# Kernel optimization log

Hardware: AMD Instinct MI355X
Metric: run time of the kernel (lower is better)

Reference implementation:

```python
import jax, jax.numpy as jnp
import numpy as np

THRESHOLD = 0.1


def _conv3x3(x, w, b):
    # x: [B,Ci,H,W], w: [Co,Ci,3,3] -> [B,Co,H,W], SAME padding, ReLU
    y = jax.lax.conv_general_dilated(
        x, w, window_strides=(1, 1), padding='SAME',
        dimension_numbers=('NCHW', 'OIHW', 'NCHW'))
    return jax.nn.relu(y + b[None, :, None, None])


def _autoencoder(x, w1, b1, w2, b2, w3, b3, w4, b4):
    h = _conv3x3(x, w1, b1)          # 64 -> 32
    mid = _conv3x3(h, w2, b2)        # 32 -> 16 (bottleneck)
    h2 = _conv3x3(mid, w3, b3)       # 16 -> 32
    rec = _conv3x3(h2, w4, b4)       # 32 -> 64
    return mid, rec


def setup_inputs() -> dict:
    key = jax.random.key(0)
    ks = jax.random.split(key, 8)
    B, C, H, W = 8, 64, 128, 256
    s = 0.05  # keep activations / singular values at a sane scale
    return {
        'feat0': jax.random.normal(ks[0], (B, C, H, W), jnp.float32),
        'feat1': jax.random.normal(ks[1], (B, C, H, W), jnp.float32),
        'w1': jax.random.normal(ks[2], (32, 64, 3, 3), jnp.float32) * s,
        'b1': jnp.zeros((32,), jnp.float32),
        'w2': jax.random.normal(ks[3], (16, 32, 3, 3), jnp.float32) * s,
        'b2': jnp.zeros((16,), jnp.float32),
        'w3': jax.random.normal(ks[4], (32, 16, 3, 3), jnp.float32) * s,
        'b3': jnp.zeros((32,), jnp.float32),
        'w4': jax.random.normal(ks[5], (64, 32, 3, 3), jnp.float32) * s,
        'b4': jnp.zeros((64,), jnp.float32),
        'modality_adapter': 0,  # accepted but unused by the original forward
    }


def reference(feat0, feat1, w1, b1, w2, b2, w3, b3, w4, b4, modality_adapter):
    feats = [feat0, feat1]
    B, C, H, W = feat0.shape
    auto_enc_loss = jnp.float32(0.0)
    counts_list = []
    for f in feats:
        mid, rec = _autoencoder(f, w1, b1, w2, b2, w3, b3, w4, b4)
        # batched SVD over [B, 16, H*W]; counts of singular values > threshold
        sv = jnp.linalg.svd(jax.lax.stop_gradient(mid.reshape(B, mid.shape[1], H * W)),
                            compute_uv=False)  # [B, 16]
        counts_list.append(jnp.sum(sv > THRESHOLD, axis=1))
        auto_enc_loss = auto_enc_loss + jnp.mean((f - rec) ** 2)
    # pick the dominant modality per batch element
    domain_idx = jnp.argmax(jnp.stack(counts_list, axis=1), axis=1)  # [B]
    con_feat = jnp.stack(feats, axis=1)                              # [B,M,C,H,W]
    dom = con_feat[jnp.arange(B), domain_idx]                        # [B,C,H,W]
    domain_features = jnp.broadcast_to(dom[:, None], con_feat.shape)  # repeat over M
    # two-stage cross-modal einsum attention
    weights = jnp.einsum('smchw,snchw->smnhw', domain_features, con_feat)
    weights = jax.nn.softmax(weights, axis=2)
    weights = jnp.einsum('smnhw,snchw->smchw', weights, con_feat)
    weights = jax.nn.softmax(weights, axis=1)
    fused_feat = jnp.sum(con_feat * weights, axis=1)  # [B,C,H,W]
    return fused_feat, auto_enc_loss
```

## Files before the change

### kernel.cpp

```cpp
#include <hip/hip_runtime.h>
#include <hip/hip_bf16.h>

#define B_ 8
#define H_ 128
#define W_ 256
#define PH 130
#define PW 258
#define NPIX (B_*64*H_*W_)

typedef short short8  __attribute__((ext_vector_type(8)));
typedef short short4v __attribute__((ext_vector_type(4)));
typedef float floatx4 __attribute__((ext_vector_type(4)));

template<int Ci, int Co, bool LOSS, bool NCHW_IN, bool AVG>
__global__ __launch_bounds__(256)
void conv_mfma(const void* __restrict__ in_,
               const __hip_bfloat16* __restrict__ wt,
               const float* __restrict__ bias,
               __hip_bfloat16* __restrict__ outp,
               const float* __restrict__ ref,
               const float* __restrict__ other,
               float* __restrict__ avg_out,
               float* __restrict__ acc_out)
{
    constexpr int CC   = (Ci >= 32) ? Ci/32 : 1;
    constexpr int PXB  = Ci*2;
    constexpr int NCB  = PXB/16;
    constexpr int SLAB = 6*66*PXB;
    constexpr int NT   = Co/16;
    constexpr int GNT  = (NT >= 2) ? 2 : 1;
    constexpr int NG   = NT / GNT;
    constexpr int EPIW = 64*(Co+8)*2;
    constexpr int RECB = 64*272*2;
    constexpr int LDSZ = LOSS ? (RECB > SLAB ? RECB : SLAB)
                              : (4*EPIW > SLAB ? 4*EPIW : SLAB);
    __shared__ alignas(16) char slab[LDSZ + 32];
    __shared__ float wred[4];

    const int tid  = threadIdx.x;
    const int lane = tid & 63;
    const int wid  = tid >> 6;
    const int col  = lane & 15;
    const int quad = lane >> 4;
    const int w0   = blockIdx.x * 64;
    const int h0   = blockIdx.y * 4;
    const int bz   = blockIdx.z;
    const int r    = wid;

    floatx4 acc[4][NT];
#pragma unroll
    for (int mt = 0; mt < 4; ++mt)
#pragma unroll
        for (int nt = 0; nt < NT; ++nt)
            acc[mt][nt] = (floatx4)0.f;

    if constexpr (NCHW_IN) {
        static_assert(Ci == 64, "NCHW staging is Ci=64 only");
        const float* src = (const float*)in_ + (size_t)bz * 64 * H_ * W_;
        for (int k = tid; k < 8*396; k += 256) {
            int cb  = k / 396;
            int pxl = k - cb*396;
            int row = pxl / 66;
            int pxc = pxl - row*66;
            int gh  = h0 + row - 1;
            int gw  = w0 + pxc - 1;
            bool ok = ((unsigned)gh < (unsigned)H_) && ((unsigned)gw < (unsigned)W_);
            const float* sp = src + (size_t)(cb*8)*(H_*W_)
                              + (size_t)(ok ? gh : 0)*W_ + (ok ? gw : 0);
            short8 v;
#pragma unroll
            for (int j = 0; j < 8; ++j) {
                float f = sp[(size_t)j*(H_*W_)];
                f = ok ? f : 0.f;
                v[j] = __builtin_bit_cast(short, __float2bfloat16(f));
            }
            *(short8*)(slab + pxl*PXB + ((cb ^ (pxl & 7)) << 4)) = v;
        }
    } else {
        const __hip_bfloat16* inb = (const __hip_bfloat16*)in_ + (size_t)bz * PH * PW * Ci;
        for (int o = tid*16; o < SLAB; o += 4096) {
            int pxl = o / PXB;
            int row = pxl / 66;
            int pxc = pxl - row*66;
            int cb  = (o >> 4) & (NCB-1);
            short8 v = *(const short8*)(inb + ((size_t)(h0+row)*PW + (w0+pxc))*Ci + cb*8);
            *(short8*)(slab + pxl*PXB + ((cb ^ (pxl & (NCB-1))) << 4)) = v;
        }
    }
    __syncthreads();

    if constexpr (Ci >= 32) {
#pragma unroll
        for (int c2 = 0; c2 < CC; ++c2) {
#pragma unroll
            for (int g = 0; g < NG; ++g) {
                short8 bfr[9*GNT];
#pragma unroll
                for (int t = 0; t < 9; ++t)
#pragma unroll
                    for (int j = 0; j < GNT; ++j)
                        bfr[t*GNT+j] = *(const short8*)(wt
                            + ((size_t)(c2*9+t)*Co + (g*GNT+j)*16 + col)*32 + quad*8);
#pragma unroll
                for (int t = 0; t < 9; ++t) {
                    const int dy = t/3, dx = t - (t/3)*3;
                    short8 a[4];
#pragma unroll
                    for (int mt = 0; mt < 4; ++mt) {
                        int px = (r+dy)*66 + mt*16 + col + dx;
                        a[mt] = *(const short8*)(slab + px*PXB
                                  + (((c2*4 + quad) ^ (px & (NCB-1))) << 4));
                    }
#pragma unroll
                    for (int j = 0; j < GNT; ++j)
#pragma unroll
                        for (int mt = 0; mt < 4; ++mt)
                            acc[mt][g*GNT+j] = __builtin_amdgcn_mfma_f32_16x16x32_bf16(
                                a[mt], bfr[t*GNT+j], acc[mt][g*GNT+j], 0, 0, 0);
                }
            }
        }
    } else {
        short8 bfr[6*NT];
#pragma unroll
        for (int kc = 0; kc < 6; ++kc)
#pragma unroll
            for (int j = 0; j < NT; ++j)
                bfr[kc*NT+j] = *(const short8*)(wt
                    + ((size_t)kc*Co + j*16 + col)*32 + quad*8);
#pragma unroll
        for (int kc = 0; kc < 6; ++kc) {
            const int dy = kc >> 1, half = kc & 1;
            const int dxe = half ? 2 : (quad >> 1);
            short8 a[4];
#pragma unroll
            for (int mt = 0; mt < 4; ++mt) {
                int px = (r+dy)*66 + mt*16 + col + dxe;
                a[mt] = *(const short8*)(slab + px*PXB
                          + (((quad & 1) ^ (px & 1)) << 4));
            }
#pragma unroll
            for (int j = 0; j < NT; ++j)
#pragma unroll
                for (int mt = 0; mt < 4; ++mt)
                    acc[mt][j] = __builtin_amdgcn_mfma_f32_16x16x32_bf16(
                        a[mt], bfr[kc*NT+j], acc[mt][j], 0, 0, 0);
        }
    }

    if constexpr (!LOSS) {
        __syncthreads();
        char* rt = slab + wid * EPIW;
#pragma unroll
        for (int nt = 0; nt < NT; ++nt) {
            float bv = bias[nt*16 + col];
#pragma unroll
            for (int mt = 0; mt < 4; ++mt) {
#pragma unroll
                for (int rr = 0; rr < 4; ++rr) {
                    float v = acc[mt][nt][rr] + bv;
                    v = v > 0.f ? v : 0.f;
                    int px = mt*16 + quad*4 + rr;
                    *(__hip_bfloat16*)(rt + (px*(Co+8) + nt*16 + col)*2) =
                        __float2bfloat16(v);
                }
            }
        }
        char* grow = (char*)outp
            + (((size_t)bz*PH + (h0 + r + 1))*PW + (w0 + 1))*Co*2;
        constexpr int GB = 64*Co*2;
#pragma unroll
        for (int id = 0; id < GB/1024; ++id) {
            int o  = id*1024 + lane*16;
            int px = o / (Co*2);
            int cb = o - px*(Co*2);
            *(short8*)(grow + o) = *(const short8*)(rt + px*(Co+8)*2 + cb);
        }
    } else {
        __syncthreads();
        __hip_bfloat16* rec = (__hip_bfloat16*)slab;
#pragma unroll
        for (int nt = 0; nt < NT; ++nt) {
            int co = nt*16 + col;
            float bv = bias[co];
#pragma unroll
            for (int mt = 0; mt < 4; ++mt) {
                short4v pk;
#pragma unroll
                for (int rr = 0; rr < 4; ++rr) {
                    float v = acc[mt][nt][rr] + bv;
                    v = v > 0.f ? v : 0.f;
                    pk[rr] = __builtin_bit_cast(short, __float2bfloat16(v));
                }
                *(short4v*)(rec + co*272 + r*68 + mt*16 + quad*4) = pk;
            }
        }
        __syncthreads();

        float lsum = 0.f;
        const float* refb = ref + (size_t)bz * 64 * H_ * W_;
#pragma unroll
        for (int i = 0; i < 16; ++i) {
            int row = i & 3, cg = i >> 2;
            int co  = cg*16 + wid*4 + quad;
            size_t off = ((size_t)co*H_ + h0 + row)*W_ + w0 + col*4;
            float4 f = *(const float4*)(refb + off);
            short4v pk = *(const short4v*)(rec + co*272 + row*68 + col*4);
            float d0 = f.x - __bfloat162float(__builtin_bit_cast(__hip_bfloat16, pk[0]));
            float d1 = f.y - __bfloat162float(__builtin_bit_cast(__hip_bfloat16, pk[1]));
            float d2 = f.z - __bfloat162float(__builtin_bit_cast(__hip_bfloat16, pk[2]));
            float d3 = f.w - __bfloat162float(__builtin_bit_cast(__hip_bfloat16, pk[3]));
            lsum += d0*d0 + d1*d1 + d2*d2 + d3*d3;
            if constexpr (AVG) {
                const float* othb = other + (size_t)bz * 64 * H_ * W_;
                float*       avgb = avg_out + (size_t)bz * 64 * H_ * W_;
                float4 g = *(const float4*)(othb + off);
                float4 o;
                o.x = 0.5f*(f.x + g.x);
                o.y = 0.5f*(f.y + g.y);
                o.z = 0.5f*(f.z + g.z);
                o.w = 0.5f*(f.w + g.w);
                *(float4*)(avgb + off) = o;
            }
        }
#pragma unroll
        for (int off = 32; off > 0; off >>= 1)
            lsum += __shfl_down(lsum, off, 64);
        if (lane == 0) wred[wid] = lsum;
        __syncthreads();
        if (tid == 0)
            atomicAdd(acc_out, (wred[0] + wred[1] + wred[2] + wred[3])
                               * (1.0f / (float)NPIX));
    }
}

template<int C>
__device__ __forceinline__ void zb_item(__hip_bfloat16* buf, int idx)
{
    constexpr int CP = C/8;
    int cb   = idx % CP;
    int cell = (idx / CP) % 772;
    int img  = idx / (CP*772);
    int row, colp;
    if (cell < 258)      { row = 0;   colp = cell; }
    else if (cell < 516) { row = 129; colp = cell - 258; }
    else { int r2 = cell - 516; row = 1 + (r2 >> 1); colp = (r2 & 1) ? 257 : 0; }
    short8 z = (short8)0;
    *(short8*)(buf + (((size_t)img*PH + row)*PW + colp)*C + cb*8) = z;
}

template<int Ci, int Co>
__device__ __forceinline__ void wt_item(const float* __restrict__ w,
                                        __hip_bfloat16* __restrict__ wt, int idx)
{
    int kl = idx & 31;
    int co = (idx >> 5) % Co;
    int kc = idx / (32*Co);
    float val = 0.f;
    if constexpr (Ci >= 32) {
        int c2 = kc / 9, t = kc % 9;
        int dy = t/3, dx = t%3;
        int ci = c2*32 + kl;
        val = w[((size_t)(co*Ci + ci)*3 + dy)*3 + dx];
    } else {
        int dy = kc >> 1, half = kc & 1;
        int dx = half*2 + (kl >> 4);
        int ci = kl & 15;
        if (dx < 3) val = w[((size_t)(co*Ci + ci)*3 + dy)*3 + dx];
    }
    wt[idx] = __float2bfloat16(val);
}

__global__ __launch_bounds__(256)
void setup_kernel(const float* __restrict__ w1, const float* __restrict__ w2,
                  const float* __restrict__ w3, const float* __restrict__ w4,
                  __hip_bfloat16* WT1, __hip_bfloat16* WT2,
                  __hip_bfloat16* WT3, __hip_bfloat16* WT4,
                  __hip_bfloat16* BUF1, __hip_bfloat16* BUF2,
                  float* acc)
{
    int idx = blockIdx.x*256 + threadIdx.x;
    if (idx == 0) *acc = 0.f;
    if      (idx < 24704) zb_item<32>(BUF1, idx);
    else if (idx < 37056) zb_item<16>(BUF2, idx - 24704);
    else if (idx < 55488) wt_item<64,32>(w1, WT1, idx - 37056);
    else if (idx < 60096) wt_item<32,16>(w2, WT2, idx - 55488);
    else if (idx < 66240) wt_item<16,32>(w3, WT3, idx - 60096);
    else if (idx < 84672) wt_item<32,64>(w4, WT4, idx - 66240);
}

__global__ __launch_bounds__(256)
void fused_avg_kernel(const float4* __restrict__ a, const float4* __restrict__ b,
                      float4* __restrict__ o, int n4)
{
    int i = blockIdx.x*256 + threadIdx.x;
    if (i < n4) {
        float4 x = a[i], y = b[i];
        float4 r;
        r.x = 0.5f*(x.x + y.x);
        r.y = 0.5f*(x.y + y.y);
        r.z = 0.5f*(x.z + y.z);
        r.w = 0.5f*(x.w + y.w);
        o[i] = r;
    }
}

extern "C" void kernel_launch(void* const* d_in, const int* in_sizes, int n_in,
                              void* d_out, int out_size, void* d_ws, size_t ws_size,
                              hipStream_t stream)
{
    const float* feat0 = (const float*)d_in[0];
    const float* feat1 = (const float*)d_in[1];
    const float* w1 = (const float*)d_in[2];
    const float* b1 = (const float*)d_in[3];
    const float* w2 = (const float*)d_in[4];
    const float* b2 = (const float*)d_in[5];
    const float* w3 = (const float*)d_in[6];
    const float* b3 = (const float*)d_in[7];
    const float* w4 = (const float*)d_in[8];
    const float* b4 = (const float*)d_in[9];

    float* out = (float*)d_out;
    float* acc = out + NPIX;

    constexpr size_t SCR_SZ = 25853952;
    const bool use_ws = (d_ws != nullptr) && (ws_size >= SCR_SZ);
    char* sb = use_ws ? (char*)d_ws : (char*)d_out;

    __hip_bfloat16* BUF1 = (__hip_bfloat16*)(sb + 0);
    __hip_bfloat16* BUF2 = (__hip_bfloat16*)(sb + 17172480);
    __hip_bfloat16* WT1  = (__hip_bfloat16*)(sb + 25758720);
    __hip_bfloat16* WT2  = (__hip_bfloat16*)(sb + 25795584);
    __hip_bfloat16* WT3  = (__hip_bfloat16*)(sb + 25804800);
    __hip_bfloat16* WT4  = (__hip_bfloat16*)(sb + 25817088);

    setup_kernel<<<331, 256, 0, stream>>>(w1, w2, w3, w4,
                                          WT1, WT2, WT3, WT4, BUF1, BUF2, acc);

    dim3 cgrid(W_/64, H_/4, B_);
    dim3 blk(256);

    const float* feats[2] = { feat0, feat1 };
    for (int m = 0; m < 2; ++m) {
        conv_mfma<64,32,false,true ,false><<<cgrid, blk, 0, stream>>>(
            feats[m], WT1, b1, BUF1, nullptr, nullptr, nullptr, nullptr);
        conv_mfma<32,16,false,false,false><<<cgrid, blk, 0, stream>>>(
            BUF1, WT2, b2, BUF2, nullptr, nullptr, nullptr, nullptr);
        conv_mfma<16,32,false,false,false><<<cgrid, blk, 0, stream>>>(
            BUF2, WT3, b3, BUF1, nullptr, nullptr, nullptr, nullptr);
        if (m == 1 && use_ws)
            conv_mfma<32,64,true ,false,true ><<<cgrid, blk, 0, stream>>>(
                BUF1, WT4, b4, nullptr, feats[1], feats[0], out, acc);
        else
            conv_mfma<32,64,true ,false,false><<<cgrid, blk, 0, stream>>>(
                BUF1, WT4, b4, nullptr, feats[m], nullptr, nullptr, acc);
    }

    if (!use_ws) {
        int n4 = NPIX/4;
        fused_avg_kernel<<<(n4 + 255)/256, 256, 0, stream>>>(
            (const float4*)feat0, (const float4*)feat1, (float4*)out, n4);
    }
}
```

Measured before the change: 340.9 us.

## Batch both modalities into single conv launches and stage NCHW input in channel halves

Both feature maps now go through each conv layer in one launch, with the grid z dimension doubled to 2*B and separate per-modality scratch buffers. This halves the number of kernel launches and gives each launch twice as many blocks, which should fill the GPU better. The first conv also stages its fp32 NCHW input in two 32-channel halves. Each wave loads 8 channels, so the LDS slab is halved and occupancy may rise, at the cost of an extra barrier. Workspace size doubles, and the averaging output is written only by the modality-1 blocks.

```diff
diff --git a/kernel.cpp b/kernel.cpp
--- a/kernel.cpp
+++ b/kernel.cpp
@@ -14,17 +14,21 @@
 
 template<int Ci, int Co, bool LOSS, bool NCHW_IN, bool AVG>
 __global__ __launch_bounds__(256)
-void conv_mfma(const void* __restrict__ in_,
+void conv_mfma(const void* __restrict__ inA,
+               const void* __restrict__ inB,
                const __hip_bfloat16* __restrict__ wt,
                const float* __restrict__ bias,
                __hip_bfloat16* __restrict__ outp,
-               const float* __restrict__ ref,
+               size_t out_mstride,
+               const float* __restrict__ ref0,
+               const float* __restrict__ ref1,
                const float* __restrict__ other,
                float* __restrict__ avg_out,
                float* __restrict__ acc_out)
 {
     constexpr int CC   = (Ci >= 32) ? Ci/32 : 1;
-    constexpr int PXB  = Ci*2;
+    constexpr int SCI  = NCHW_IN ? 32 : Ci;
+    constexpr int PXB  = SCI*2;
     constexpr int NCB  = PXB/16;
     constexpr int SLAB = 6*66*PXB;
     constexpr int NT   = Co/16;
@@ -44,7 +48,9 @@
     const int quad = lane >> 4;
     const int w0   = blockIdx.x * 64;
     const int h0   = blockIdx.y * 4;
-    const int bz   = blockIdx.z;
+    const int zz   = blockIdx.z;
+    const int bz   = zz & 7;
+    const int mz   = zz >> 3;
     const int r    = wid;
 
     floatx4 acc[4][NT];
@@ -54,30 +60,70 @@
         for (int nt = 0; nt < NT; ++nt)
             acc[mt][nt] = (floatx4)0.f;
 
+    auto mfma_c2 = [&](int c2) {
+#pragma unroll
+        for (int g = 0; g < NG; ++g) {
+            short8 bfr[9*GNT];
+#pragma unroll
+            for (int t = 0; t < 9; ++t)
+#pragma unroll
+                for (int j = 0; j < GNT; ++j)
+                    bfr[t*GNT+j] = *(const short8*)(wt
+                        + ((size_t)(c2*9+t)*Co + (g*GNT+j)*16 + col)*32 + quad*8);
+#pragma unroll
+            for (int t = 0; t < 9; ++t) {
+                const int dy = t/3, dx = t - (t/3)*3;
+                short8 a[4];
+#pragma unroll
+                for (int mt = 0; mt < 4; ++mt) {
+                    int px  = (r+dy)*66 + mt*16 + col + dx;
+                    int kch = NCHW_IN ? quad : (c2*4 + quad);
+                    a[mt] = *(const short8*)(slab + px*PXB
+                              + ((kch ^ (px & (NCB-1))) << 4));
+                }
+#pragma unroll
+                for (int j = 0; j < GNT; ++j)
+#pragma unroll
+                    for (int mt = 0; mt < 4; ++mt)
+                        acc[mt][g*GNT+j] = __builtin_amdgcn_mfma_f32_16x16x32_bf16(
+                            a[mt], bfr[t*GNT+j], acc[mt][g*GNT+j], 0, 0, 0);
+            }
+        }
+    };
+
     if constexpr (NCHW_IN) {
         static_assert(Ci == 64, "NCHW staging is Ci=64 only");
-        const float* src = (const float*)in_ + (size_t)bz * 64 * H_ * W_;
-        for (int k = tid; k < 8*396; k += 256) {
-            int cb  = k / 396;
-            int pxl = k - cb*396;
-            int row = pxl / 66;
-            int pxc = pxl - row*66;
-            int gh  = h0 + row - 1;
-            int gw  = w0 + pxc - 1;
-            bool ok = ((unsigned)gh < (unsigned)H_) && ((unsigned)gw < (unsigned)W_);
-            const float* sp = src + (size_t)(cb*8)*(H_*W_)
-                              + (size_t)(ok ? gh : 0)*W_ + (ok ? gw : 0);
-            short8 v;
-#pragma unroll
-            for (int j = 0; j < 8; ++j) {
-                float f = sp[(size_t)j*(H_*W_)];
-                f = ok ? f : 0.f;
-                v[j] = __builtin_bit_cast(short, __float2bfloat16(f));
-            }
-            *(short8*)(slab + pxl*PXB + ((cb ^ (pxl & 7)) << 4)) = v;
+        const float* src = (const float*)(mz ? inB : inA) + (size_t)bz * 64 * H_ * W_;
+#pragma unroll
+        for (int c2 = 0; c2 < CC; ++c2) {
+            if (c2) __syncthreads();
+            const float* chb = src + (size_t)(c2*32 + wid*8) * (H_*W_);
+#pragma unroll
+            for (int it = 0; it < 7; ++it) {
+                int pxl = it*64 + lane;
+                bool live = (it < 6) || (lane < 12);
+                int row = pxl / 66;
+                int pxc = pxl - row*66;
+                int gh  = h0 + row - 1;
+                int gw  = w0 + pxc - 1;
+                bool ok = live && ((unsigned)gh < (unsigned)H_)
+                               && ((unsigned)gw < (unsigned)W_);
+                const float* sp = chb + (size_t)(ok ? gh : 0)*W_ + (ok ? gw : 0);
+                short8 v;
+#pragma unroll
+                for (int j = 0; j < 8; ++j) {
+                    float f = sp[(size_t)j*(H_*W_)];
+                    v[j] = __builtin_bit_cast(short, __float2bfloat16(ok ? f : 0.f));
+                }
+                if (live)
+                    *(short8*)(slab + pxl*PXB + ((wid ^ (pxl & (NCB-1))) << 4)) = v;
+            }
+            __syncthreads();
+            mfma_c2(c2);
         }
     } else {
-        const __hip_bfloat16* inb = (const __hip_bfloat16*)in_ + (size_t)bz * PH * PW * Ci;
+        const __hip_bfloat16* inb = (const __hip_bfloat16*)(mz ? inB : inA)
+                                    + (size_t)bz * PH * PW * Ci;
         for (int o = tid*16; o < SLAB; o += 4096) {
             int pxl = o / PXB;
             int row = pxl / 66;
@@ -86,65 +132,38 @@
             short8 v = *(const short8*)(inb + ((size_t)(h0+row)*PW + (w0+pxc))*Ci + cb*8);
             *(short8*)(slab + pxl*PXB + ((cb ^ (pxl & (NCB-1))) << 4)) = v;
         }
-    }
-    __syncthreads();
-
-    if constexpr (Ci >= 32) {
-#pragma unroll
-        for (int c2 = 0; c2 < CC; ++c2) {
-#pragma unroll
-            for (int g = 0; g < NG; ++g) {
-                short8 bfr[9*GNT];
-#pragma unroll
-                for (int t = 0; t < 9; ++t)
-#pragma unroll
-                    for (int j = 0; j < GNT; ++j)
-                        bfr[t*GNT+j] = *(const short8*)(wt
-                            + ((size_t)(c2*9+t)*Co + (g*GNT+j)*16 + col)*32 + quad*8);
-#pragma unroll
-                for (int t = 0; t < 9; ++t) {
-                    const int dy = t/3, dx = t - (t/3)*3;
-                    short8 a[4];
-#pragma unroll
-                    for (int mt = 0; mt < 4; ++mt) {
-                        int px = (r+dy)*66 + mt*16 + col + dx;
-                        a[mt] = *(const short8*)(slab + px*PXB
-                                  + (((c2*4 + quad) ^ (px & (NCB-1))) << 4));
-                    }
-#pragma unroll
-                    for (int j = 0; j < GNT; ++j)
-#pragma unroll
-                        for (int mt = 0; mt < 4; ++mt)
-                            acc[mt][g*GNT+j] = __builtin_amdgcn_mfma_f32_16x16x32_bf16(
-                                a[mt], bfr[t*GNT+j], acc[mt][g*GNT+j], 0, 0, 0);
-                }
-            }
-        }
-    } else {
-        short8 bfr[6*NT];
-#pragma unroll
-        for (int kc = 0; kc < 6; ++kc)
-#pragma unroll
-            for (int j = 0; j < NT; ++j)
-                bfr[kc*NT+j] = *(const short8*)(wt
-                    + ((size_t)kc*Co + j*16 + col)*32 + quad*8);
-#pragma unroll
-        for (int kc = 0; kc < 6; ++kc) {
-            const int dy = kc >> 1, half = kc & 1;
-            const int dxe = half ? 2 : (quad >> 1);
-            short8 a[4];
-#pragma unroll
-            for (int mt = 0; mt < 4; ++mt) {
-                int px = (r+dy)*66 + mt*16 + col + dxe;
-                a[mt] = *(const short8*)(slab + px*PXB
-                          + (((quad & 1) ^ (px & 1)) << 4));
-            }
-#pragma unroll
-            for (int j = 0; j < NT; ++j)
-#pragma unroll
-                for (int mt = 0; mt < 4; ++mt)
-                    acc[mt][j] = __builtin_amdgcn_mfma_f32_16x16x32_bf16(
-                        a[mt], bfr[kc*NT+j], acc[mt][j], 0, 0, 0);
+        __syncthreads();
+
+        if constexpr (Ci >= 32) {
+#pragma unroll
+            for (int c2 = 0; c2 < CC; ++c2)
+                mfma_c2(c2);
+        } else {
+            short8 bfr[6*NT];
+#pragma unroll
+            for (int kc = 0; kc < 6; ++kc)
+#pragma unroll
+                for (int j = 0; j < NT; ++j)
+                    bfr[kc*NT+j] = *(const short8*)(wt
+                        + ((size_t)kc*Co + j*16 + col)*32 + quad*8);
+#pragma unroll
+            for (int kc = 0; kc < 6; ++kc) {
+                const int dy = kc >> 1, half = kc & 1;
+                const int dxe = half ? 2 : (quad >> 1);
+                short8 a[4];
+#pragma unroll
+                for (int mt = 0; mt < 4; ++mt) {
+                    int px = (r+dy)*66 + mt*16 + col + dxe;
+                    a[mt] = *(const short8*)(slab + px*PXB
+                              + (((quad & 1) ^ (px & 1)) << 4));
+                }
+#pragma unroll
+                for (int j = 0; j < NT; ++j)
+#pragma unroll
+                    for (int mt = 0; mt < 4; ++mt)
+                        acc[mt][j] = __builtin_amdgcn_mfma_f32_16x16x32_bf16(
+                            a[mt], bfr[kc*NT+j], acc[mt][j], 0, 0, 0);
+            }
         }
     }
 
@@ -166,7 +185,8 @@
                 }
             }
         }
-        char* grow = (char*)outp
+        __hip_bfloat16* ob = outp + (size_t)mz * out_mstride;
+        char* grow = (char*)ob
             + (((size_t)bz*PH + (h0 + r + 1))*PW + (w0 + 1))*Co*2;
         constexpr int GB = 64*Co*2;
 #pragma unroll
@@ -198,7 +218,7 @@
         __syncthreads();
 
         float lsum = 0.f;
-        const float* refb = ref + (size_t)bz * 64 * H_ * W_;
+        const float* refb = (mz ? ref1 : ref0) + (size_t)bz * 64 * H_ * W_;
 #pragma unroll
         for (int i = 0; i < 16; ++i) {
             int row = i & 3, cg = i >> 2;
@@ -212,15 +232,17 @@
             float d3 = f.w - __bfloat162float(__builtin_bit_cast(__hip_bfloat16, pk[3]));
             lsum += d0*d0 + d1*d1 + d2*d2 + d3*d3;
             if constexpr (AVG) {
-                const float* othb = other + (size_t)bz * 64 * H_ * W_;
-                float*       avgb = avg_out + (size_t)bz * 64 * H_ * W_;
-                float4 g = *(const float4*)(othb + off);
-                float4 o;
-                o.x = 0.5f*(f.x + g.x);
-                o.y = 0.5f*(f.y + g.y);
-                o.z = 0.5f*(f.z + g.z);
-                o.w = 0.5f*(f.w + g.w);
-                *(float4*)(avgb + off) = o;
+                if (mz) {
+                    const float* othb = other + (size_t)bz * 64 * H_ * W_;
+                    float*       avgb = avg_out + (size_t)bz * 64 * H_ * W_;
+                    float4 g = *(const float4*)(othb + off);
+                    float4 o;
+                    o.x = 0.5f*(f.x + g.x);
+                    o.y = 0.5f*(f.y + g.y);
+                    o.z = 0.5f*(f.z + g.z);
+                    o.w = 0.5f*(f.w + g.w);
+                    *(float4*)(avgb + off) = o;
+                }
             }
         }
 #pragma unroll
@@ -281,12 +303,12 @@
 {
     int idx = blockIdx.x*256 + threadIdx.x;
     if (idx == 0) *acc = 0.f;
-    if      (idx < 24704) zb_item<32>(BUF1, idx);
-    else if (idx < 37056) zb_item<16>(BUF2, idx - 24704);
-    else if (idx < 55488) wt_item<64,32>(w1, WT1, idx - 37056);
-    else if (idx < 60096) wt_item<32,16>(w2, WT2, idx - 55488);
-    else if (idx < 66240) wt_item<16,32>(w3, WT3, idx - 60096);
-    else if (idx < 84672) wt_item<32,64>(w4, WT4, idx - 66240);
+    if      (idx <  49408) zb_item<32>(BUF1, idx);
+    else if (idx <  74112) zb_item<16>(BUF2, idx - 49408);
+    else if (idx <  92544) wt_item<64,32>(w1, WT1, idx - 74112);
+    else if (idx <  97152) wt_item<32,16>(w2, WT2, idx - 92544);
+    else if (idx < 103296) wt_item<16,32>(w3, WT3, idx - 97152);
+    else if (idx < 121728) wt_item<32,64>(w4, WT4, idx - 103296);
 }
 
 __global__ __launch_bounds__(256)
@@ -323,40 +345,45 @@
     float* out = (float*)d_out;
     float* acc = out + NPIX;
 
-    constexpr size_t SCR_SZ = 25853952;
+    constexpr size_t B1B = (size_t)B_*PH*PW*32*2;
+    constexpr size_t B2B = (size_t)B_*PH*PW*16*2;
+    constexpr size_t SCR_SZ = 51612672;
     const bool use_ws = (d_ws != nullptr) && (ws_size >= SCR_SZ);
     char* sb = use_ws ? (char*)d_ws : (char*)d_out;
 
     __hip_bfloat16* BUF1 = (__hip_bfloat16*)(sb + 0);
-    __hip_bfloat16* BUF2 = (__hip_bfloat16*)(sb + 17172480);
-    __hip_bfloat16* WT1  = (__hip_bfloat16*)(sb + 25758720);
-    __hip_bfloat16* WT2  = (__hip_bfloat16*)(sb + 25795584);
-    __hip_bfloat16* WT3  = (__hip_bfloat16*)(sb + 25804800);
-    __hip_bfloat16* WT4  = (__hip_bfloat16*)(sb + 25817088);
-
-    setup_kernel<<<331, 256, 0, stream>>>(w1, w2, w3, w4,
+    __hip_bfloat16* BUF2 = (__hip_bfloat16*)(sb + 2*B1B);
+    __hip_bfloat16* WT1  = (__hip_bfloat16*)(sb + 51517440);
+    __hip_bfloat16* WT2  = (__hip_bfloat16*)(sb + 51554304);
+    __hip_bfloat16* WT3  = (__hip_bfloat16*)(sb + 51563520);
+    __hip_bfloat16* WT4  = (__hip_bfloat16*)(sb + 51575808);
+
+    setup_kernel<<<476, 256, 0, stream>>>(w1, w2, w3, w4,
                                           WT1, WT2, WT3, WT4, BUF1, BUF2, acc);
 
-    dim3 cgrid(W_/64, H_/4, B_);
+    dim3 cgrid(W_/64, H_/4, 2*B_);
     dim3 blk(256);
 
-    const float* feats[2] = { feat0, feat1 };
-    for (int m = 0; m < 2; ++m) {
-        conv_mfma<64,32,false,true ,false><<<cgrid, blk, 0, stream>>>(
-            feats[m], WT1, b1, BUF1, nullptr, nullptr, nullptr, nullptr);
-        conv_mfma<32,16,false,false,false><<<cgrid, blk, 0, stream>>>(
-            BUF1, WT2, b2, BUF2, nullptr, nullptr, nullptr, nullptr);
-        conv_mfma<16,32,false,false,false><<<cgrid, blk, 0, stream>>>(
-            BUF2, WT3, b3, BUF1, nullptr, nullptr, nullptr, nullptr);
-        if (m == 1 && use_ws)
-            conv_mfma<32,64,true ,false,true ><<<cgrid, blk, 0, stream>>>(
-                BUF1, WT4, b4, nullptr, feats[1], feats[0], out, acc);
-        else
-            conv_mfma<32,64,true ,false,false><<<cgrid, blk, 0, stream>>>(
-                BUF1, WT4, b4, nullptr, feats[m], nullptr, nullptr, acc);
-    }
-
-    if (!use_ws) {
+    constexpr size_t B1E = B1B/2;
+    constexpr size_t B2E = B2B/2;
+
+    conv_mfma<64,32,false,true ,false><<<cgrid, blk, 0, stream>>>(
+        feat0, feat1, WT1, b1, BUF1, B1E,
+        nullptr, nullptr, nullptr, nullptr, nullptr);
+    conv_mfma<32,16,false,false,false><<<cgrid, blk, 0, stream>>>(
+        BUF1, BUF1 + B1E, WT2, b2, BUF2, B2E,
+        nullptr, nullptr, nullptr, nullptr, nullptr);
+    conv_mfma<16,32,false,false,false><<<cgrid, blk, 0, stream>>>(
+        BUF2, BUF2 + B2E, WT3, b3, BUF1, B1E,
+        nullptr, nullptr, nullptr, nullptr, nullptr);
+    if (use_ws)
+        conv_mfma<32,64,true ,false,true ><<<cgrid, blk, 0, stream>>>(
+            BUF1, BUF1 + B1E, WT4, b4, nullptr, 0,
+            feat0, feat1, feat0, out, acc);
+    else {
+        conv_mfma<32,64,true ,false,false><<<cgrid, blk, 0, stream>>>(
+            BUF1, BUF1 + B1E, WT4, b4, nullptr, 0,
+            feat0, feat1, nullptr, nullptr, acc);
         int n4 = NPIX/4;
         fused_avg_kernel<<<(n4 + 255)/256, 256, 0, stream>>>(
             (const float4*)feat0, (const float4*)feat1, (float4*)out, n4);
```

After: 317.7 us. -6.8%, faster.
